# Optimization experiments

Hardware: AMD Instinct MI355X
Metric: run time of the kernel (lower is better)

The kernel has to match this reference:

```python
import jax, jax.numpy as jnp
import numpy as np
import math

PS = 65          # patch_size
NB_ANG = 8       # num_ang_bins
NB_SP = 4        # num_spatial_bins
CLIP = 0.2
EPS = 1e-10
BIN_KS = 2 * (PS // (NB_SP + 1))   # 26
BIN_STRIDE = PS // NB_SP           # 16
BIN_PAD = BIN_KS // 4              # 6


def _gaussian_kernel2d(ks, sigma):
    x = jnp.arange(ks, dtype=jnp.float32) - ks // 2
    if ks % 2 == 0:
        x = x + 0.5
    g = jnp.exp(-(x * x) / (2.0 * sigma * sigma))
    g = g / g.sum()
    return jnp.outer(g, g)  # [ps, ps]


def _sift_pooling_kernel(ks):
    ks2 = ks / 2.0
    xc2 = ks2 - jnp.abs(jnp.arange(ks, dtype=jnp.float32) + 0.5 - ks2)
    return jnp.outer(xc2, xc2) / (ks2 * ks2)  # [26, 26] triangular bilinear kernel


def _l2n(x):
    # torch F.normalize(p=2, dim=-1, eps=1e-12)
    return x / jnp.maximum(jnp.linalg.norm(x, axis=-1, keepdims=True), 1e-12)


def setup_inputs() -> dict:
    key = jax.random.key(0)
    image_batch = jax.random.uniform(key, (16, 3, 520, 520), dtype=jnp.float32)
    return {"image_batch": image_batch}


def reference(image_batch):
    B, C, H, W = image_batch.shape
    nH, nW = H // PS, W // PS
    # torch unfold(2,ps,ps).unfold(3,ps,ps).reshape(-1, c, ps, ps)
    # (row-major reshape replicated exactly, including its channel/patch mixing)
    p = image_batch.reshape(B, C, nH, PS, nW, PS).transpose(0, 1, 2, 4, 3, 5)
    x = p.reshape(-1, C, PS, PS)  # [N, C, ps, ps]; (N,C) treated as independent patches
    N = x.shape[0]

    # kornia spatial_gradient(mode='diff', normalized=True): replicate pad, central diff / 2
    xp = jnp.pad(x, ((0, 0), (0, 0), (1, 1), (1, 1)), mode='edge')
    gx = (xp[:, :, 1:-1, 2:] - xp[:, :, 1:-1, :-2]) * 0.5
    gy = (xp[:, :, 2:, 1:-1] - xp[:, :, :-2, 1:-1]) * 0.5

    mag = jnp.sqrt(gx * gx + gy * gy + EPS)
    ori = jnp.arctan2(gy, gx + EPS) + 2.0 * jnp.pi
    gk = _gaussian_kernel2d(PS, PS / math.sqrt(2.0))
    mag = mag * gk  # Gaussian spatial weighting

    # soft orientation binning
    o_big = (NB_ANG / (2.0 * jnp.pi)) * ori
    bo0f = jnp.floor(o_big)
    wo1 = o_big - bo0f
    bo0 = (bo0f % NB_ANG).astype(jnp.int32)
    bo1 = (bo0 + 1) % NB_ANG
    # [N, C, ps, ps, 8] soft histogram field
    contrib = (jax.nn.one_hot(bo0, NB_ANG, dtype=x.dtype) * ((1.0 - wo1) * mag)[..., None]
               + jax.nn.one_hot(bo1, NB_ANG, dtype=x.dtype) * (wo1 * mag)[..., None])

    # spatial pooling: conv 26x26, stride 16, zero-pad 6 -> 4x4 per angle bin
    contrib = jnp.moveaxis(contrib, -1, 2).reshape(N * C * NB_ANG, 1, PS, PS)
    pk = _sift_pooling_kernel(BIN_KS)[None, None]  # [1,1,26,26]
    pooled = jax.lax.conv_general_dilated(
        contrib, pk,
        window_strides=(BIN_STRIDE, BIN_STRIDE),
        padding=((BIN_PAD, BIN_PAD), (BIN_PAD, BIN_PAD)),
        dimension_numbers=('NCHW', 'OIHW', 'NCHW'))  # [N*C*8, 1, 4, 4]

    desc = pooled.reshape(N, C, NB_ANG * NB_SP * NB_SP)  # [N, C, 128]
    desc = _l2n(desc)
    desc = jnp.clip(desc, 0.0, CLIP)
    desc = _l2n(desc)
    return desc  # [B*nH*nW, C, 128] (root_sift=False)
```

## Files before the change

kernel.cpp:

```cpp
#include <hip/hip_runtime.h>
#include <math.h>

#define PSTR 33

__device__ __forceinline__ float fast_atan2f(float y, float x) {
    float ax = fabsf(x), ay = fabsf(y);
    float mx = fmaxf(ax, ay);
    float mn = fminf(ax, ay);
    float a = mn * __builtin_amdgcn_rcpf(fmaxf(mx, 1e-30f));
    float s = a * a;
    float r = fmaf(s, fmaf(s, fmaf(s, fmaf(s, fmaf(s, -0.0117212f, 0.05265332f),
                    -0.11643287f), 0.19354346f), -0.33262347f), 0.99997726f) * a;
    r = (ay > ax) ? (1.57079637f - r) : r;
    r = (x < 0.0f) ? (3.14159274f - r) : r;
    return copysignf(r, y);
}

template<int CTRL>
__device__ __forceinline__ float upd_dpp(float old, float src) {
    return __uint_as_float((unsigned)__builtin_amdgcn_update_dpp(
        (int)__float_as_uint(old), (int)__float_as_uint(src), CTRL, 0xF, 0xF, false));
}

#define WGT(SY, RR) ((13.0f - fabsf((float)(RR) - 16.0f * (SY) - 6.5f)) * (1.0f / 13.0f))

#define FMA8(P, W)                                                        \
    P##0 = fmaf(s0, (W), P##0); P##1 = fmaf(s1, (W), P##1);               \
    P##2 = fmaf(s2, (W), P##2); P##3 = fmaf(s3, (W), P##3);               \
    P##4 = fmaf(s4, (W), P##4); P##5 = fmaf(s5, (W), P##5);               \
    P##6 = fmaf(s6, (W), P##6); P##7 = fmaf(s7, (W), P##7);

#define RDL(RR)  __uint_as_float((unsigned)__builtin_amdgcn_readlane((int)__float_as_uint(G),   (RR)))
#define RDLC(RR) __uint_as_float((unsigned)__builtin_amdgcn_readlane((int)__float_as_uint(C64), (RR)))

#define PIX(ARR, I, RR, ACCUM)                                            \
    {                                                                     \
        float grow = ((RR) < 64) ? RDL((RR) & 63) : g64;                  \
        float gw = grow * GC;                                             \
        float c64r = ((RR) < 64) ? RDLC((RR) & 63) : c64top;              \
        float xc = ARR[I];                                                \
        float xl = upd_dpp<0x138>(xc, xc);                                \
        float xr = upd_dpp<0x130>(c64r, xc);                              \
        float dx = xr - xl;                                               \
        float dy = ARR[(I) + 1] - ARR[(I) - 1];                           \
        float ax_ = fabsf(dx), ay_ = fabsf(dy);                           \
        float mx = fmaxf(fmaxf(ax_, ay_), 1e-30f);                        \
        float mn = fminf(ax_, ay_);                                       \
        float t = mn * __builtin_amdgcn_rcpf(mx);                         \
        float ts = t * t;                                                 \
        float f = fmaf(ts, fmaf(ts, fmaf(ts, fmaf(ts, fmaf(ts,           \
                  -0.01492344f, 0.06703556f), -0.14824473f), 0.24642112f),\
                  -0.42350443f), 1.27321063f) * t;                        \
        float magw = sqrtf(fmaf(dx, dx, fmaf(dy, dy, 4e-10f))) * gw;      \
        bool sdb = ay_ > ax_;                                             \
        bool sxb = dx < 0.0f;                                             \
        bool syb = dy < 0.0f;                                             \
        bool midb = sxb != syb;                                           \
        bool parb = sdb != midb;                                          \
        float wo1 = parb ? (1.0f - f) : f;                                \
        float q1 = wo1 * magw;                                            \
        float q0 = magw - q1;                                             \
        bool h0 = !syb && !midb && !parb;                                 \
        bool h1 = !syb && !midb &&  parb;                                 \
        bool h2 = !syb &&  midb && !parb;                                 \
        bool h3 = !syb &&  midb &&  parb;                                 \
        bool h4 =  syb && !midb && !parb;                                 \
        bool h5 =  syb && !midb &&  parb;                                 \
        bool h6 =  syb &&  midb && !parb;                                 \
        bool h7 =  syb &&  midb &&  parb;                                 \
        float s0 = h0 ? q0 : (h7 ? q1 : 0.0f);                            \
        float s1 = h1 ? q0 : (h0 ? q1 : 0.0f);                            \
        float s2 = h2 ? q0 : (h1 ? q1 : 0.0f);                            \
        float s3 = h3 ? q0 : (h2 ? q1 : 0.0f);                            \
        float s4 = h4 ? q0 : (h3 ? q1 : 0.0f);                            \
        float s5 = h5 ? q0 : (h4 ? q1 : 0.0f);                            \
        float s6 = h6 ? q0 : (h5 ? q1 : 0.0f);                            \
        float s7 = h7 ? q0 : (h6 ? q1 : 0.0f);                            \
        ACCUM                                                             \
    }

#define LOAD_RA(BASE)                                                     \
    _Pragma("unroll")                                                     \
    for (int i = 0; i < 18; ++i) {                                        \
        int rr = (BASE) + i; rr = (rr < 0) ? 0 : ((rr > 64) ? 64 : rr);   \
        RA[i] = src[rr * 520 + lane];                                     \
    }
#define LOAD_RB(BASE)                                                     \
    _Pragma("unroll")                                                     \
    for (int i = 0; i < 19; ++i) {                                        \
        int rr = (BASE) + i; rr = (rr < 0) ? 0 : ((rr > 64) ? 64 : rr);   \
        RB[i] = src[rr * 520 + lane];                                     \
    }
#define PIN_RA  _Pragma("unroll") for (int i = 0; i < 18; ++i) asm volatile("" : "+v"(RA[i]));
#define PIN_RB  _Pragma("unroll") for (int i = 0; i < 19; ++i) asm volatile("" : "+v"(RB[i]));

__global__ __launch_bounds__(64)
__attribute__((amdgpu_waves_per_eu(2, 3)))
void sift_kernel(const float* __restrict__ in, float* __restrict__ out) {
    __shared__ float part[65 * PSTR];
    __shared__ float c64buf[67];

    const int lane = threadIdx.x;
    const int m  = blockIdx.x;
    const int bc = m >> 6;
    const int ij = m & 63;
    const float* src = in + (size_t)bc * (520 * 520) + (ij >> 3) * (65 * 520) + (ij & 7) * 65;

    {
        int rr = lane - 1; rr = (rr < 0) ? 0 : rr;
        c64buf[lane] = src[rr * 520 + 64];
        if (lane < 3) {
            int r2 = 63 + lane; r2 = (r2 > 64) ? 64 : r2;
            c64buf[64 + lane] = src[r2 * 520 + 64];
        }
        if (lane < 32) part[64 * PSTR + lane] = 0.0f;
    }
    float C64    = src[lane * 520 + 64];
    float c64top = src[64 * 520 + 64];
    float xl63   = src[lane * 520 + 63];
    float xl63b  = src[64 * 520 + 63];

    float RA[18], RB[19];
    LOAD_RA(-1)
    LOAD_RB(15)

    float dd = (float)(lane - 32);
    float E  = __expf(-(dd * dd) * (1.0f / 4225.0f));
    float ssum = E;
    #pragma unroll
    for (int off = 32; off > 0; off >>= 1) ssum += __shfl_xor(ssum, off, 64);
    const float e64 = __expf(-1024.0f / 4225.0f);
    float inv = 1.0f / (ssum + e64);
    float G   = E * inv;
    float g64 = e64 * inv;
    const float GC = 0.5f * G;

    const int cb = lane * PSTR;

    float A0=0,A1=0,A2=0,A3=0,A4=0,A5=0,A6=0,A7=0;
    float B0=0,B1=0,B2=0,B3=0,B4=0,B5=0,B6=0,B7=0;
    float C0=0,C1=0,C2=0,C3=0,C4=0,C5=0,C6=0,C7=0;
    float F0=0,F1=0,F2=0,F3=0,F4=0,F5=0,F6=0,F7=0;

    PIN_RA
    #pragma unroll
    for (int r = 0; r < 10; ++r)   PIX(RA, r + 1, r, FMA8(A, WGT(0, r)))
    #pragma unroll
    for (int r = 10; r < 16; ++r)  PIX(RA, r + 1, r, FMA8(A, WGT(0, r)) FMA8(B, WGT(1, r)))

    LOAD_RA(31)
    PIN_RB
    #pragma unroll
    for (int r = 16; r < 20; ++r)  PIX(RB, r - 15, r, FMA8(A, WGT(0, r)) FMA8(B, WGT(1, r)))
    #pragma unroll
    for (int r = 20; r < 26; ++r)  PIX(RB, r - 15, r, FMA8(B, WGT(1, r)))
    #pragma unroll
    for (int r = 26; r < 32; ++r)  PIX(RB, r - 15, r, FMA8(B, WGT(1, r)) FMA8(C, WGT(2, r)))
    part[cb + 0] = A0; part[cb + 1] = A1; part[cb + 2] = A2; part[cb + 3] = A3;
    part[cb + 4] = A4; part[cb + 5] = A5; part[cb + 6] = A6; part[cb + 7] = A7;

    LOAD_RB(47)
    PIN_RA
    #pragma unroll
    for (int r = 32; r < 36; ++r)  PIX(RA, r - 31, r, FMA8(B, WGT(1, r)) FMA8(C, WGT(2, r)))
    #pragma unroll
    for (int r = 36; r < 42; ++r)  PIX(RA, r - 31, r, FMA8(C, WGT(2, r)))
    #pragma unroll
    for (int r = 42; r < 48; ++r)  PIX(RA, r - 31, r, FMA8(C, WGT(2, r)) FMA8(F, WGT(3, r)))
    part[cb + 8] = B0; part[cb + 9] = B1; part[cb +10] = B2; part[cb +11] = B3;
    part[cb +12] = B4; part[cb +13] = B5; part[cb +14] = B6; part[cb +15] = B7;

    PIN_RB
    #pragma unroll
    for (int r = 48; r < 52; ++r)  PIX(RB, r - 47, r, FMA8(C, WGT(2, r)) FMA8(F, WGT(3, r)))
    #pragma unroll
    for (int r = 52; r < 65; ++r)  PIX(RB, r - 47, r, FMA8(F, WGT(3, r)))
    part[cb +16] = C0; part[cb +17] = C1; part[cb +18] = C2; part[cb +19] = C3;
    part[cb +20] = C4; part[cb +21] = C5; part[cb +22] = C6; part[cb +23] = C7;
    part[cb +24] = F0; part[cb +25] = F1; part[cb +26] = F2; part[cb +27] = F3;
    part[cb +28] = F4; part[cb +29] = F5; part[cb +30] = F6; part[cb +31] = F7;

    {
        int r = lane;
        float xu  = c64buf[r];
        float xcc = c64buf[r + 1];
        float xd  = c64buf[r + 2];
        float dx = xcc - xl63;
        float dy = xd - xu;
        float magw = sqrtf(fmaf(dx, dx, fmaf(dy, dy, 4e-10f))) * (G * (0.5f * g64));
        float ang = fast_atan2f(dy, dx + 2e-10f);
        float o   = fmaf(ang, 1.27323954f, 8.0f);
        int bi = (int)o;
        float wo1 = o - (float)bi;
        int b0 = bi & 7;
        int b1 = (bi + 1) & 7;
        float q1 = wo1 * magw;
        float q0 = magw - q1;
        float* eb = &part[64 * PSTR];
        int syA = (r + 6) >> 4; if (syA > 3) syA = 3;
        float uA = (float)(r - 16 * syA + 6);
        float wA = (13.0f - fabsf(uA - 12.5f)) * (1.0f / 13.0f);
        atomicAdd(eb + syA * 8 + b0, q0 * wA);
        atomicAdd(eb + syA * 8 + b1, q1 * wA);
        int syB = syA - 1;
        if (syB >= 0) {
            float uB = (float)(r - 16 * syB + 6);
            float wB = (13.0f - fabsf(uB - 12.5f)) * (1.0f / 13.0f);
            if (wB > 0.0f) {
                atomicAdd(eb + syB * 8 + b0, q0 * wB);
                atomicAdd(eb + syB * 8 + b1, q1 * wB);
            }
        }
        if (lane == 0) {
            float xu2  = c64buf[64];
            float xc2  = c64buf[65];
            float xd2  = c64buf[66];
            float dx2 = xc2 - xl63b;
            float dy2 = xd2 - xu2;
            float mg = sqrtf(fmaf(dx2, dx2, fmaf(dy2, dy2, 4e-10f))) * (g64 * (0.5f * g64));
            float an = fast_atan2f(dy2, dx2 + 2e-10f);
            float o2 = fmaf(an, 1.27323954f, 8.0f);
            int bi2 = (int)o2;
            float w1 = o2 - (float)bi2;
            int c0 = bi2 & 7;
            int c1 = (bi2 + 1) & 7;
            float p1 = w1 * mg;
            float p0 = mg - p1;
            const float w64 = 3.5f * (1.0f / 13.0f);
            atomicAdd(eb + 3 * 8 + c0, p0 * w64);
            atomicAdd(eb + 3 * 8 + c1, p1 * w64);
        }
    }

    {
        float v0, v1;
        #pragma unroll
        for (int h = 0; h < 2; ++h) {
            int o  = lane + h * 64;
            int a  = o >> 4;
            int sy = (o >> 2) & 3;
            int sx = o & 3;
            float s = 0.0f;
            #pragma unroll 2
            for (int k = 0; k < 26; ++k) {
                int c = sx * 16 - 6 + k;
                if ((unsigned)c <= 64u) {
                    float wc = (13.0f - fabsf((float)k - 12.5f)) * (1.0f / 13.0f);
                    s = fmaf(wc, part[c * PSTR + sy * 8 + a], s);
                }
            }
            if (h == 0) v0 = s; else v1 = s;
        }
        float ss = v0 * v0 + v1 * v1;
        #pragma unroll
        for (int off = 32; off > 0; off >>= 1) ss += __shfl_xor(ss, off, 64);
        float sc = 1.0f / fmaxf(sqrtf(ss), 1e-12f);
        v0 = fminf(fmaxf(v0 * sc, 0.0f), 0.2f);
        v1 = fminf(fmaxf(v1 * sc, 0.0f), 0.2f);
        ss = v0 * v0 + v1 * v1;
        #pragma unroll
        for (int off = 32; off > 0; off >>= 1) ss += __shfl_xor(ss, off, 64);
        sc = 1.0f / fmaxf(sqrtf(ss), 1e-12f);
        out[(size_t)m * 128 + lane]      = v0 * sc;
        out[(size_t)m * 128 + lane + 64] = v1 * sc;
    }
}

extern "C" void kernel_launch(void* const* d_in, const int* in_sizes, int n_in,
                              void* d_out, int out_size, void* d_ws, size_t ws_size,
                              hipStream_t stream) {
    const float* in = (const float*)d_in[0];
    float* out = (float*)d_out;
    sift_kernel<<<3072, 64, 0, stream>>>(in, out);
}
```

Baseline: 41.20 us.

## Loop over 16-row bands with one register buffer and LDS atomic accumulation

Replaces the fully unrolled 65-row sweep, which used two register row buffers and 32 live accumulators, with a non-unrolled loop over four 16-row bands. Each band reloads 18 rows into one buffer, keeps 24 accumulators, and adds its partial bin sums into shared memory with atomic adds. Row 64 is handled in a separate tail block. This cuts register pressure and code size, but adds LDS atomics, a zero-fill of the whole partial buffer, and serialized per-band loads with less overlap between loading and compute.

```diff
diff --git a/kernel.cpp b/kernel.cpp
--- a/kernel.cpp
+++ b/kernel.cpp
@@ -22,7 +22,9 @@
         (int)__float_as_uint(old), (int)__float_as_uint(src), CTRL, 0xF, 0xF, false));
 }
 
-#define WGT(SY, RR) ((13.0f - fabsf((float)(RR) - 16.0f * (SY) - 6.5f)) * (1.0f / 13.0f))
+__device__ __forceinline__ float rdlane_f(float x, int l) {
+    return __uint_as_float((unsigned)__builtin_amdgcn_readlane((int)__float_as_uint(x), l));
+}
 
 #define FMA8(P, W)                                                        \
     P##0 = fmaf(s0, (W), P##0); P##1 = fmaf(s1, (W), P##1);               \
@@ -30,19 +32,21 @@
     P##4 = fmaf(s4, (W), P##4); P##5 = fmaf(s5, (W), P##5);               \
     P##6 = fmaf(s6, (W), P##6); P##7 = fmaf(s7, (W), P##7);
 
-#define RDL(RR)  __uint_as_float((unsigned)__builtin_amdgcn_readlane((int)__float_as_uint(G),   (RR)))
-#define RDLC(RR) __uint_as_float((unsigned)__builtin_amdgcn_readlane((int)__float_as_uint(C64), (RR)))
-
-#define PIX(ARR, I, RR, ACCUM)                                            \
+#define WA(K) ((3.5f - (float)(K)) * (1.0f / 13.0f))
+#define WB(K) ((13.0f - fabsf((float)(K) - 6.5f)) * (1.0f / 13.0f))
+#define WC(K) (((float)(K) - 9.5f) * (1.0f / 13.0f))
+
+#define PIX(K, ACCUM)                                                     \
     {                                                                     \
-        float grow = ((RR) < 64) ? RDL((RR) & 63) : g64;                  \
+        int row_ = rowb + (K);                                            \
+        float grow = rdlane_f(G, row_);                                   \
         float gw = grow * GC;                                             \
-        float c64r = ((RR) < 64) ? RDLC((RR) & 63) : c64top;              \
-        float xc = ARR[I];                                                \
+        float c64r = rdlane_f(C64, row_);                                 \
+        float xc = R[(K) + 1];                                            \
         float xl = upd_dpp<0x138>(xc, xc);                                \
         float xr = upd_dpp<0x130>(c64r, xc);                              \
         float dx = xr - xl;                                               \
-        float dy = ARR[(I) + 1] - ARR[(I) - 1];                           \
+        float dy = R[(K) + 2] - R[(K)];                                   \
         float ax_ = fabsf(dx), ay_ = fabsf(dy);                           \
         float mx = fmaxf(fmaxf(ax_, ay_), 1e-30f);                        \
         float mn = fminf(ax_, ay_);                                       \
@@ -79,21 +83,6 @@
         ACCUM                                                             \
     }
 
-#define LOAD_RA(BASE)                                                     \
-    _Pragma("unroll")                                                     \
-    for (int i = 0; i < 18; ++i) {                                        \
-        int rr = (BASE) + i; rr = (rr < 0) ? 0 : ((rr > 64) ? 64 : rr);   \
-        RA[i] = src[rr * 520 + lane];                                     \
-    }
-#define LOAD_RB(BASE)                                                     \
-    _Pragma("unroll")                                                     \
-    for (int i = 0; i < 19; ++i) {                                        \
-        int rr = (BASE) + i; rr = (rr < 0) ? 0 : ((rr > 64) ? 64 : rr);   \
-        RB[i] = src[rr * 520 + lane];                                     \
-    }
-#define PIN_RA  _Pragma("unroll") for (int i = 0; i < 18; ++i) asm volatile("" : "+v"(RA[i]));
-#define PIN_RB  _Pragma("unroll") for (int i = 0; i < 19; ++i) asm volatile("" : "+v"(RB[i]));
-
 __global__ __launch_bounds__(64)
 __attribute__((amdgpu_waves_per_eu(2, 3)))
 void sift_kernel(const float* __restrict__ in, float* __restrict__ out) {
@@ -106,6 +95,8 @@
     const int ij = m & 63;
     const float* src = in + (size_t)bc * (520 * 520) + (ij >> 3) * (65 * 520) + (ij & 7) * 65;
 
+    for (int k = lane; k < 65 * PSTR; k += 64) part[k] = 0.0f;
+
     {
         int rr = lane - 1; rr = (rr < 0) ? 0 : rr;
         c64buf[lane] = src[rr * 520 + 64];
@@ -113,16 +104,11 @@
             int r2 = 63 + lane; r2 = (r2 > 64) ? 64 : r2;
             c64buf[64 + lane] = src[r2 * 520 + 64];
         }
-        if (lane < 32) part[64 * PSTR + lane] = 0.0f;
     }
     float C64    = src[lane * 520 + 64];
     float c64top = src[64 * 520 + 64];
     float xl63   = src[lane * 520 + 63];
     float xl63b  = src[64 * 520 + 63];
-
-    float RA[18], RB[19];
-    LOAD_RA(-1)
-    LOAD_RB(15)
 
     float dd = (float)(lane - 32);
     float E  = __expf(-(dd * dd) * (1.0f / 4225.0f));
@@ -137,48 +123,78 @@
 
     const int cb = lane * PSTR;
 
-    float A0=0,A1=0,A2=0,A3=0,A4=0,A5=0,A6=0,A7=0;
-    float B0=0,B1=0,B2=0,B3=0,B4=0,B5=0,B6=0,B7=0;
-    float C0=0,C1=0,C2=0,C3=0,C4=0,C5=0,C6=0,C7=0;
-    float F0=0,F1=0,F2=0,F3=0,F4=0,F5=0,F6=0,F7=0;
-
-    PIN_RA
-    #pragma unroll
-    for (int r = 0; r < 10; ++r)   PIX(RA, r + 1, r, FMA8(A, WGT(0, r)))
-    #pragma unroll
-    for (int r = 10; r < 16; ++r)  PIX(RA, r + 1, r, FMA8(A, WGT(0, r)) FMA8(B, WGT(1, r)))
-
-    LOAD_RA(31)
-    PIN_RB
-    #pragma unroll
-    for (int r = 16; r < 20; ++r)  PIX(RB, r - 15, r, FMA8(A, WGT(0, r)) FMA8(B, WGT(1, r)))
-    #pragma unroll
-    for (int r = 20; r < 26; ++r)  PIX(RB, r - 15, r, FMA8(B, WGT(1, r)))
-    #pragma unroll
-    for (int r = 26; r < 32; ++r)  PIX(RB, r - 15, r, FMA8(B, WGT(1, r)) FMA8(C, WGT(2, r)))
-    part[cb + 0] = A0; part[cb + 1] = A1; part[cb + 2] = A2; part[cb + 3] = A3;
-    part[cb + 4] = A4; part[cb + 5] = A5; part[cb + 6] = A6; part[cb + 7] = A7;
-
-    LOAD_RB(47)
-    PIN_RA
-    #pragma unroll
-    for (int r = 32; r < 36; ++r)  PIX(RA, r - 31, r, FMA8(B, WGT(1, r)) FMA8(C, WGT(2, r)))
-    #pragma unroll
-    for (int r = 36; r < 42; ++r)  PIX(RA, r - 31, r, FMA8(C, WGT(2, r)))
-    #pragma unroll
-    for (int r = 42; r < 48; ++r)  PIX(RA, r - 31, r, FMA8(C, WGT(2, r)) FMA8(F, WGT(3, r)))
-    part[cb + 8] = B0; part[cb + 9] = B1; part[cb +10] = B2; part[cb +11] = B3;
-    part[cb +12] = B4; part[cb +13] = B5; part[cb +14] = B6; part[cb +15] = B7;
-
-    PIN_RB
-    #pragma unroll
-    for (int r = 48; r < 52; ++r)  PIX(RB, r - 47, r, FMA8(C, WGT(2, r)) FMA8(F, WGT(3, r)))
-    #pragma unroll
-    for (int r = 52; r < 65; ++r)  PIX(RB, r - 47, r, FMA8(F, WGT(3, r)))
-    part[cb +16] = C0; part[cb +17] = C1; part[cb +18] = C2; part[cb +19] = C3;
-    part[cb +20] = C4; part[cb +21] = C5; part[cb +22] = C6; part[cb +23] = C7;
-    part[cb +24] = F0; part[cb +25] = F1; part[cb +26] = F2; part[cb +27] = F3;
-    part[cb +28] = F4; part[cb +29] = F5; part[cb +30] = F6; part[cb +31] = F7;
+    float R[18];
+
+    #pragma unroll 1
+    for (int b = 0; b < 4; ++b) {
+        const int rowb = b << 4;
+
+        #pragma unroll
+        for (int i = 0; i < 18; ++i) {
+            int rr = rowb - 1 + i;
+            rr = (rr < 0) ? 0 : rr;
+            R[i] = src[rr * 520 + lane];
+        }
+        #pragma unroll
+        for (int i = 0; i < 18; ++i) asm volatile("" : "+v"(R[i]));
+
+        float A0=0,A1=0,A2=0,A3=0,A4=0,A5=0,A6=0,A7=0;
+        float B0=0,B1=0,B2=0,B3=0,B4=0,B5=0,B6=0,B7=0;
+        float C0=0,C1=0,C2=0,C3=0,C4=0,C5=0,C6=0,C7=0;
+
+        #pragma unroll
+        for (int k = 0; k <= 3; ++k)   PIX(k, FMA8(A, WA(k)) FMA8(B, WB(k)))
+        #pragma unroll
+        for (int k = 4; k <= 9; ++k)   PIX(k, FMA8(B, WB(k)))
+        #pragma unroll
+        for (int k = 10; k <= 15; ++k) PIX(k, FMA8(B, WB(k)) FMA8(C, WC(k)))
+
+        if (b > 0) {
+            float* p = &part[cb + (b - 1) * 8];
+            atomicAdd(p + 0, A0); atomicAdd(p + 1, A1); atomicAdd(p + 2, A2); atomicAdd(p + 3, A3);
+            atomicAdd(p + 4, A4); atomicAdd(p + 5, A5); atomicAdd(p + 6, A6); atomicAdd(p + 7, A7);
+        }
+        {
+            float* p = &part[cb + b * 8];
+            atomicAdd(p + 0, B0); atomicAdd(p + 1, B1); atomicAdd(p + 2, B2); atomicAdd(p + 3, B3);
+            atomicAdd(p + 4, B4); atomicAdd(p + 5, B5); atomicAdd(p + 6, B6); atomicAdd(p + 7, B7);
+        }
+        if (b < 3) {
+            float* p = &part[cb + (b + 1) * 8];
+            atomicAdd(p + 0, C0); atomicAdd(p + 1, C1); atomicAdd(p + 2, C2); atomicAdd(p + 3, C3);
+            atomicAdd(p + 4, C4); atomicAdd(p + 5, C5); atomicAdd(p + 6, C6); atomicAdd(p + 7, C7);
+        }
+    }
+
+    {
+        float xc = R[17];
+        float xl = upd_dpp<0x138>(xc, xc);
+        float xr = upd_dpp<0x130>(c64top, xc);
+        float dx = xr - xl;
+        float dy = R[17] - R[16];
+        float ax_ = fabsf(dx), ay_ = fabsf(dy);
+        float mx = fmaxf(fmaxf(ax_, ay_), 1e-30f);
+        float mn = fminf(ax_, ay_);
+        float t = mn * __builtin_amdgcn_rcpf(mx);
+        float ts = t * t;
+        float f = fmaf(ts, fmaf(ts, fmaf(ts, fmaf(ts, fmaf(ts,
+                  -0.01492344f, 0.06703556f), -0.14824473f), 0.24642112f),
+                  -0.42350443f), 1.27321063f) * t;
+        float magw = sqrtf(fmaf(dx, dx, fmaf(dy, dy, 4e-10f))) * (g64 * GC);
+        bool sdb = ay_ > ax_;
+        bool sxb = dx < 0.0f;
+        bool syb = dy < 0.0f;
+        bool midb = sxb != syb;
+        bool parb = sdb != midb;
+        float wo1 = parb ? (1.0f - f) : f;
+        float q1 = wo1 * magw;
+        float q0 = magw - q1;
+        int bn0 = (syb ? 4 : 0) + (midb ? 2 : 0) + (parb ? 1 : 0);
+        int bn1 = (bn0 + 1) & 7;
+        const float W = 3.5f * (1.0f / 13.0f);
+        atomicAdd(&part[cb + 24 + bn0], q0 * W);
+        atomicAdd(&part[cb + 24 + bn1], q1 * W);
+    }
 
     {
         int r = lane;
```

Result: slower. 102.8 us (+149.5%).
